# Kernel tuning notes

Measured on AMD Instinct MI355X. Metric: run time of the kernel, lower is better.

Reference implementation:

```python
import jax, jax.numpy as jnp
import numpy as np

N_NODES = 50000


def gcn_conv(x, W, b, src, dst):
    # PyG GCNConv: lin (no bias) -> add self-loops -> symmetric deg norm ->
    # scatter-add messages to target nodes -> add bias.
    n = x.shape[0]
    xw = x @ W  # [N, H]
    loops = jnp.arange(n, dtype=src.dtype)
    s = jnp.concatenate([src, loops])
    d = jnp.concatenate([dst, loops])
    deg = jax.ops.segment_sum(jnp.ones(d.shape[0], dtype=x.dtype), d, num_segments=n)
    dinv = deg ** -0.5  # deg >= 1 due to self-loops
    norm = dinv[s] * dinv[d]  # [E+N]
    msg = xw[s] * norm[:, None]  # gather + scale, [E+N, H]
    out = jax.ops.segment_sum(msg, d, num_segments=n)  # scatter-add
    return out + b


def setup_inputs() -> dict:
    key = jax.random.key(0)
    ks = jax.random.split(key, 8)
    in_feats, hidden, out_feats, p = 64, 64, 32, 4
    x = jax.random.normal(ks[0], (N_NODES, in_feats), dtype=jnp.float32)
    edge_index = jax.random.randint(ks[1], (2, 800000), 0, N_NODES, dtype=jnp.int64)
    s1 = (1.0 / in_feats) ** 0.5
    s2 = (1.0 / hidden) ** 0.5
    W1 = jax.random.uniform(ks[2], (in_feats, hidden), jnp.float32, -s1, s1)
    b1 = jnp.zeros((hidden,), jnp.float32)
    W2 = jax.random.uniform(ks[3], (hidden, hidden), jnp.float32, -s2, s2)
    b2 = jnp.zeros((hidden,), jnp.float32)
    Wr = jax.random.uniform(ks[4], (hidden, out_feats * p), jnp.float32, -s2, s2)
    br = jax.random.uniform(ks[5], (out_feats * p,), jnp.float32, -s2, s2)
    return {"x": x, "edge_index": edge_index, "W1": W1, "b1": b1,
            "W2": W2, "b2": b2, "Wr": Wr, "br": br}


def reference(x, edge_index, W1, b1, W2, b2, Wr, br):
    src, dst = edge_index[0], edge_index[1]
    h = jax.nn.relu(gcn_conv(x, W1, b1, src, dst))
    h = jax.nn.relu(gcn_conv(h, W2, b2, src, dst))
    g = jnp.mean(h, axis=0, keepdims=True)  # [1, hidden]
    out = (g @ Wr + br).reshape(32, 4)  # (out_feats, p)
    return out
```

## Files before the change

kernel.cpp:

```cpp
#include <hip/hip_runtime.h>
#include <math.h>


#define CH 4096
#define MAXNB 1024

__global__ __launch_bounds__(256) void k_bucket_hist(const int* __restrict__ dst,
                                                     int* __restrict__ histmat,
                                                     int E, int NB) {
    __shared__ int ih[MAXNB];
    int t = threadIdx.x;
    for (int k = t; k < NB; k += 256) ih[k] = 0;
    __syncthreads();
    int base = blockIdx.x * CH;
    for (int i = 0; i < CH; i += 256) {
        int e = base + i + t;
        if (e < E) atomicAdd(&ih[dst[e] >> 6], 1);
    }
    __syncthreads();
    for (int k = t; k < NB; k += 256) histmat[(size_t)blockIdx.x * NB + k] = ih[k];
}

__global__ __launch_bounds__(256) void k_colscan(int* __restrict__ histmat,
                                                 int* __restrict__ tot,
                                                 int NB, int nch) {
    int k = blockIdx.x * 256 + threadIdx.x;
    if (k >= NB) return;
    int run = 0;
    int b = 0;
    for (; b + 8 <= nch; b += 8) {
        int v[8];
#pragma unroll
        for (int u = 0; u < 8; u++) v[u] = histmat[(size_t)(b + u) * NB + k];
#pragma unroll
        for (int u = 0; u < 8; u++) {
            int x = v[u];
            histmat[(size_t)(b + u) * NB + k] = run;
            run += x;
        }
    }
    for (; b < nch; b++) {
        int x = histmat[(size_t)b * NB + k];
        histmat[(size_t)b * NB + k] = run;
        run += x;
    }
    tot[k] = run;
}

__global__ __launch_bounds__(256) void k_scanb(const int* __restrict__ tot,
                                               int* __restrict__ bstart,
                                               int* __restrict__ offsets,
                                               int NB, int E, int n) {
    __shared__ int sc[256];
    __shared__ int carry;
    int t = threadIdx.x;
    if (t == 0) carry = 0;
    __syncthreads();
    int nchunk = (NB + 255) / 256;
    for (int c = 0; c < nchunk; c++) {
        int idx = c * 256 + t;
        int v = (idx < NB) ? tot[idx] : 0;
        sc[t] = v;
        __syncthreads();
        for (int off = 1; off < 256; off <<= 1) {
            int x = (t >= off) ? sc[t - off] : 0;
            __syncthreads();
            sc[t] += x;
            __syncthreads();
        }
        if (idx < NB) bstart[idx] = sc[t] - v + carry;
        __syncthreads();
        if (t == 0) carry += sc[255];
        __syncthreads();
    }
    if (t == 0) { bstart[NB] = E; offsets[n] = E; }
}

__global__ __launch_bounds__(256) void k_bucket_scatter(const int* __restrict__ src,
                                                        const int* __restrict__ dst,
                                                        const int* __restrict__ histmat,
                                                        const int* __restrict__ bstart,
                                                        int* __restrict__ staged,
                                                        int E, int NB) {
    __shared__ int cur[MAXNB];
    int t = threadIdx.x;
    for (int k = t; k < NB; k += 256)
        cur[k] = bstart[k] + histmat[(size_t)blockIdx.x * NB + k];
    __syncthreads();
    int base = blockIdx.x * CH;
    for (int i = 0; i < CH; i += 256) {
        int e = base + i + t;
        if (e < E) {
            int d = dst[e];
            int pos = atomicAdd(&cur[d >> 6], 1);
            staged[pos] = (src[e] << 6) | (d & 63);
        }
    }
}

__global__ __launch_bounds__(256) void k_local_sort(const int* __restrict__ staged,
                                                    const int* __restrict__ bstart,
                                                    int* __restrict__ csr_src,
                                                    int* __restrict__ offsets,
                                                    float* __restrict__ dinv, int n) {
    __shared__ int cnt[64];
    __shared__ int pos[64];
    __shared__ int cur[64];
    int t = threadIdx.x;
    if (t < 64) cnt[t] = 0;
    __syncthreads();
    int k = blockIdx.x;
    int beg = bstart[k], end = bstart[k + 1];
    for (int e = beg + t; e < end; e += 256) atomicAdd(&cnt[staged[e] & 63], 1);
    __syncthreads();
    if (t == 0) {
        int run = 0;
        for (int i = 0; i < 64; i++) { pos[i] = run; run += cnt[i]; }
    }
    __syncthreads();
    if (t < 64) {
        cur[t] = pos[t];
        int node = k * 64 + t;
        if (node < n) {
            offsets[node] = beg + pos[t];
            dinv[node] = 1.0f / sqrtf((float)(cnt[t] + 1));
        }
    }
    __syncthreads();
    for (int e = beg + t; e < end; e += 256) {
        int pk = staged[e];
        int p = atomicAdd(&cur[pk & 63], 1);
        csr_src[beg + p] = pk >> 6;
    }
}

__global__ __launch_bounds__(256) void k_gemm_scale(const float* __restrict__ X,
                                                    const float* __restrict__ W,
                                                    const float* __restrict__ dinv,
                                                    float* __restrict__ Y, int n) {
    __shared__ float Ws[64 * 64];
    __shared__ float xs[16][64];
    int t = threadIdx.x, w = t >> 6, f = t & 63;
    const float4* W4 = (const float4*)W;
    float4* Ws4 = (float4*)Ws;
#pragma unroll
    for (int j = 0; j < 4; j++) Ws4[t + 256 * j] = W4[t + 256 * j];
    int r0 = blockIdx.x * 16;
#pragma unroll
    for (int i = 0; i < 4; i++) {
        int r = r0 + w * 4 + i;
        xs[w * 4 + i][f] = (r < n) ? X[(size_t)r * 64 + f] : 0.f;
    }
    __syncthreads();
    float acc[4] = {0.f, 0.f, 0.f, 0.f};
#pragma unroll 8
    for (int k = 0; k < 64; k++) {
        float wv = Ws[k * 64 + f];
#pragma unroll
        for (int i = 0; i < 4; i++) acc[i] += xs[w * 4 + i][k] * wv;
    }
#pragma unroll
    for (int i = 0; i < 4; i++) {
        int r = r0 + w * 4 + i;
        if (r < n) Y[(size_t)r * 64 + f] = dinv[r] * acc[i];
    }
}

template <bool POOL>
__global__ __launch_bounds__(256) void k_aggregate(const float* __restrict__ Y,
                                                   const float* __restrict__ dinv,
                                                   const float* __restrict__ bias,
                                                   const int* __restrict__ offsets,
                                                   const int* __restrict__ csr_src,
                                                   float* __restrict__ H,
                                                   float* __restrict__ pbuf, int n) {
    __shared__ float4 sm4[4][16];
    const float4* Y4 = (const float4*)Y;
    int t = threadIdx.x, w = t >> 6, l = t & 63;
    int q = l >> 4, c = l & 15;
    int node = blockIdx.x * 4 + w;
    bool valid = node < n;
    float4 hval = make_float4(0.f, 0.f, 0.f, 0.f);
    if (valid) {
        float4 acc = make_float4(0.f, 0.f, 0.f, 0.f);
        if (q == 0) acc = Y4[(size_t)node * 16 + c];
        int beg = offsets[node], end = offsets[node + 1];
        for (int j = beg + q; j < end; j += 16) {
#pragma unroll
            for (int u = 0; u < 4; u++) {
                int jj = j + 4 * u;
                bool ok = jj < end;
                float4 v = make_float4(0.f, 0.f, 0.f, 0.f);
                if (ok) {
                    int s = csr_src[jj];
                    v = Y4[(size_t)s * 16 + c];
                }
                acc.x += v.x; acc.y += v.y; acc.z += v.z; acc.w += v.w;
            }
        }
#pragma unroll
        for (int m = 16; m <= 32; m <<= 1) {
            acc.x += __shfl_xor(acc.x, m);
            acc.y += __shfl_xor(acc.y, m);
            acc.z += __shfl_xor(acc.z, m);
            acc.w += __shfl_xor(acc.w, m);
        }
        float dv = dinv[node];
        float4 b4 = ((const float4*)bias)[c];
        hval.x = fmaxf(dv * acc.x + b4.x, 0.f);
        hval.y = fmaxf(dv * acc.y + b4.y, 0.f);
        hval.z = fmaxf(dv * acc.z + b4.z, 0.f);
        hval.w = fmaxf(dv * acc.w + b4.w, 0.f);
        if (!POOL && q == 0) ((float4*)H)[(size_t)node * 16 + c] = hval;
    }
    if (POOL) {
        if (q == 0) sm4[w][c] = valid ? hval : make_float4(0.f, 0.f, 0.f, 0.f);
        __syncthreads();
        if (t < 16) {
            float4 a = sm4[0][t], b = sm4[1][t], d = sm4[2][t], e = sm4[3][t];
            float4 s;
            s.x = (a.x + b.x) + (d.x + e.x);
            s.y = (a.y + b.y) + (d.y + e.y);
            s.z = (a.z + b.z) + (d.z + e.z);
            s.w = (a.w + b.w) + (d.w + e.w);
            ((float4*)pbuf)[(size_t)blockIdx.x * 16 + t] = s;
        }
    }
}

__global__ void k_mean_final(const float* __restrict__ pbuf, float* __restrict__ g,
                             int nrows) {
    __shared__ float part[256];
    int t = threadIdx.x, w = t >> 6, f = t & 63;
    float local = 0.f;
    for (int r = blockIdx.x * 4 + w; r < nrows; r += gridDim.x * 4)
        local += pbuf[(size_t)r * 64 + f];
    part[t] = local;
    __syncthreads();
    if (w == 0) {
        float tot = part[f] + part[64 + f] + part[128 + f] + part[192 + f];
        atomicAdd(&g[f], tot);
    }
}

__global__ void k_readout(const float* __restrict__ g, const float* __restrict__ Wr,
                          const float* __restrict__ br, float* __restrict__ out,
                          float invn) {
    __shared__ float gl[64];
    int t = threadIdx.x;
    if (t < 64) gl[t] = g[t] * invn;
    __syncthreads();
    float acc = br[t];
#pragma unroll
    for (int k = 0; k < 64; k++) acc += gl[k] * Wr[k * 128 + t];
    out[t] = acc;
}

extern "C" void kernel_launch(void* const* d_in, const int* in_sizes, int n_in,
                              void* d_out, int out_size, void* d_ws, size_t ws_size,
                              hipStream_t stream) {
    const float* x  = (const float*)d_in[0];
    const int*   ei = (const int*)d_in[1];
    const float* W1 = (const float*)d_in[2];
    const float* b1 = (const float*)d_in[3];
    const float* W2 = (const float*)d_in[4];
    const float* b2 = (const float*)d_in[5];
    const float* Wr = (const float*)d_in[6];
    const float* br = (const float*)d_in[7];
    float* out = (float*)d_out;

    int n = in_sizes[0] / 64;
    int E = in_sizes[1] / 2;
    const int* src = ei;
    const int* dst = ei + E;

    int NB  = (n + 63) / 64;
    int nch = (E + CH - 1) / CH;

    char* p = (char*)d_ws;
    float* y = (float*)p;      p += (size_t)n * 64 * sizeof(float);
    float* h = (float*)p;      p += (size_t)n * 64 * sizeof(float);
    float* dinv = (float*)p;   p += (size_t)n * sizeof(float);
    float* g = (float*)p;      p += 64 * sizeof(float);
    int* staged = (int*)p;     p += (size_t)E * sizeof(int);
    int* csr_src = (int*)p;    p += (size_t)E * sizeof(int);
    int* offsets = (int*)p;    p += (size_t)(n + 1) * sizeof(int);
    int* histmat = (int*)p;    p += (size_t)nch * NB * sizeof(int);
    int* tot = (int*)p;        p += (size_t)NB * sizeof(int);
    int* bstart = (int*)p;     p += (size_t)(NB + 1) * sizeof(int);

    int gb = (n + 3) / 4;

    hipMemsetAsync(g, 0, 64 * sizeof(float), stream);
    k_bucket_hist<<<nch, 256, 0, stream>>>(dst, histmat, E, NB);
    k_colscan<<<(NB + 255) / 256, 256, 0, stream>>>(histmat, tot, NB, nch);
    k_scanb<<<1, 256, 0, stream>>>(tot, bstart, offsets, NB, E, n);
    k_bucket_scatter<<<nch, 256, 0, stream>>>(src, dst, histmat, bstart, staged, E, NB);
    k_local_sort<<<NB, 256, 0, stream>>>(staged, bstart, csr_src, offsets, dinv, n);

    k_gemm_scale<<<(n + 15) / 16, 256, 0, stream>>>(x, W1, dinv, y, n);
    k_aggregate<false><<<gb, 256, 0, stream>>>(y, dinv, b1, offsets, csr_src, h, nullptr, n);
    k_gemm_scale<<<(n + 15) / 16, 256, 0, stream>>>(h, W2, dinv, y, n);
    float* pbuf = h;
    k_aggregate<true><<<gb, 256, 0, stream>>>(y, dinv, b2, offsets, csr_src, nullptr, pbuf, n);

    k_mean_final<<<64, 256, 0, stream>>>(pbuf, g, gb);
    k_readout<<<1, 128, 0, stream>>>(g, Wr, br, out, 1.0f / (float)n);
}
```

Before: 231.6 us.

## Store node features in bf16 and CSR source indices as 16-bit

Intermediate feature matrices (scaled GEMM outputs and layer-1 hidden activations) are now stored as bf16 instead of fp32, while accumulation stays in fp32. CSR source indices are narrowed to 16-bit unsigned shorts. This halves the bytes moved by the gather-heavy aggregation and by the GEMM loads and stores. The cost is lost precision, and the 16-bit indices cannot represent node ids above 65535; since the later shift by 6 keeps only 16 bits, correctness depends on n staying below 65536.

```diff
diff --git a/kernel.cpp b/kernel.cpp
--- a/kernel.cpp
+++ b/kernel.cpp
@@ -4,6 +4,14 @@
 
 #define CH 4096
 #define MAXNB 1024
+
+__device__ __forceinline__ float bf2f(unsigned short u) {
+    return __uint_as_float(((unsigned)u) << 16);
+}
+__device__ __forceinline__ unsigned short f2bf(float x) {
+    unsigned b = __float_as_uint(x);
+    return (unsigned short)((b + 0x7FFF + ((b >> 16) & 1)) >> 16);
+}
 
 __global__ __launch_bounds__(256) void k_bucket_hist(const int* __restrict__ dst,
                                                      int* __restrict__ histmat,
@@ -100,7 +108,7 @@
 
 __global__ __launch_bounds__(256) void k_local_sort(const int* __restrict__ staged,
                                                     const int* __restrict__ bstart,
-                                                    int* __restrict__ csr_src,
+                                                    unsigned short* __restrict__ csr,
                                                     int* __restrict__ offsets,
                                                     float* __restrict__ dinv, int n) {
     __shared__ int cnt[64];
@@ -130,14 +138,15 @@
     for (int e = beg + t; e < end; e += 256) {
         int pk = staged[e];
         int p = atomicAdd(&cur[pk & 63], 1);
-        csr_src[beg + p] = pk >> 6;
-    }
-}
-
-__global__ __launch_bounds__(256) void k_gemm_scale(const float* __restrict__ X,
+        csr[beg + p] = (unsigned short)(pk >> 6);
+    }
+}
+
+template <bool BIN>
+__global__ __launch_bounds__(256) void k_gemm_scale(const void* __restrict__ Xv,
                                                     const float* __restrict__ W,
                                                     const float* __restrict__ dinv,
-                                                    float* __restrict__ Y, int n) {
+                                                    unsigned short* __restrict__ Y, int n) {
     __shared__ float Ws[64 * 64];
     __shared__ float xs[16][64];
     int t = threadIdx.x, w = t >> 6, f = t & 63;
@@ -149,7 +158,11 @@
 #pragma unroll
     for (int i = 0; i < 4; i++) {
         int r = r0 + w * 4 + i;
-        xs[w * 4 + i][f] = (r < n) ? X[(size_t)r * 64 + f] : 0.f;
+        float v = 0.f;
+        if (r < n)
+            v = BIN ? bf2f(((const unsigned short*)Xv)[(size_t)r * 64 + f])
+                    : ((const float*)Xv)[(size_t)r * 64 + f];
+        xs[w * 4 + i][f] = v;
     }
     __syncthreads();
     float acc[4] = {0.f, 0.f, 0.f, 0.f};
@@ -162,20 +175,20 @@
 #pragma unroll
     for (int i = 0; i < 4; i++) {
         int r = r0 + w * 4 + i;
-        if (r < n) Y[(size_t)r * 64 + f] = dinv[r] * acc[i];
+        if (r < n) Y[(size_t)r * 64 + f] = f2bf(dinv[r] * acc[i]);
     }
 }
 
 template <bool POOL>
-__global__ __launch_bounds__(256) void k_aggregate(const float* __restrict__ Y,
+__global__ __launch_bounds__(256) void k_aggregate(const unsigned short* __restrict__ Y,
                                                    const float* __restrict__ dinv,
                                                    const float* __restrict__ bias,
                                                    const int* __restrict__ offsets,
-                                                   const int* __restrict__ csr_src,
-                                                   float* __restrict__ H,
+                                                   const unsigned short* __restrict__ csr,
+                                                   unsigned short* __restrict__ H,
                                                    float* __restrict__ pbuf, int n) {
     __shared__ float4 sm4[4][16];
-    const float4* Y4 = (const float4*)Y;
+    const ushort4* Y4 = (const ushort4*)Y;
     int t = threadIdx.x, w = t >> 6, l = t & 63;
     int q = l >> 4, c = l & 15;
     int node = blockIdx.x * 4 + w;
@@ -183,19 +196,21 @@
     float4 hval = make_float4(0.f, 0.f, 0.f, 0.f);
     if (valid) {
         float4 acc = make_float4(0.f, 0.f, 0.f, 0.f);
-        if (q == 0) acc = Y4[(size_t)node * 16 + c];
+        if (q == 0) {
+            ushort4 u = Y4[(size_t)node * 16 + c];
+            acc = make_float4(bf2f(u.x), bf2f(u.y), bf2f(u.z), bf2f(u.w));
+        }
         int beg = offsets[node], end = offsets[node + 1];
         for (int j = beg + q; j < end; j += 16) {
 #pragma unroll
             for (int u = 0; u < 4; u++) {
                 int jj = j + 4 * u;
-                bool ok = jj < end;
-                float4 v = make_float4(0.f, 0.f, 0.f, 0.f);
-                if (ok) {
-                    int s = csr_src[jj];
-                    v = Y4[(size_t)s * 16 + c];
+                if (jj < end) {
+                    int s = csr[jj];
+                    ushort4 v = Y4[(size_t)s * 16 + c];
+                    acc.x += bf2f(v.x); acc.y += bf2f(v.y);
+                    acc.z += bf2f(v.z); acc.w += bf2f(v.w);
                 }
-                acc.x += v.x; acc.y += v.y; acc.z += v.z; acc.w += v.w;
             }
         }
 #pragma unroll
@@ -211,7 +226,12 @@
         hval.y = fmaxf(dv * acc.y + b4.y, 0.f);
         hval.z = fmaxf(dv * acc.z + b4.z, 0.f);
         hval.w = fmaxf(dv * acc.w + b4.w, 0.f);
-        if (!POOL && q == 0) ((float4*)H)[(size_t)node * 16 + c] = hval;
+        if (!POOL && q == 0) {
+            ushort4 o;
+            o.x = f2bf(hval.x); o.y = f2bf(hval.y);
+            o.z = f2bf(hval.z); o.w = f2bf(hval.w);
+            ((ushort4*)H)[(size_t)node * 16 + c] = o;
+        }
     }
     if (POOL) {
         if (q == 0) sm4[w][c] = valid ? hval : make_float4(0.f, 0.f, 0.f, 0.f);
@@ -278,31 +298,30 @@
     int nch = (E + CH - 1) / CH;
 
     char* p = (char*)d_ws;
-    float* y = (float*)p;      p += (size_t)n * 64 * sizeof(float);
-    float* h = (float*)p;      p += (size_t)n * 64 * sizeof(float);
+    unsigned short* y1 = (unsigned short*)p; p += (size_t)n * 64 * sizeof(unsigned short);
+    unsigned short* y2 = (unsigned short*)p; p += (size_t)n * 64 * sizeof(unsigned short);
+    float* pbuf = (float*)p;   p += (size_t)((n + 3) / 4) * 64 * sizeof(float);
     float* dinv = (float*)p;   p += (size_t)n * sizeof(float);
     float* g = (float*)p;      p += 64 * sizeof(float);
     int* staged = (int*)p;     p += (size_t)E * sizeof(int);
-    int* csr_src = (int*)p;    p += (size_t)E * sizeof(int);
     int* offsets = (int*)p;    p += (size_t)(n + 1) * sizeof(int);
     int* histmat = (int*)p;    p += (size_t)nch * NB * sizeof(int);
     int* tot = (int*)p;        p += (size_t)NB * sizeof(int);
     int* bstart = (int*)p;     p += (size_t)(NB + 1) * sizeof(int);
-
-    int gb = (n + 3) / 4;
+    unsigned short* csr = (unsigned short*)p; p += (size_t)E * sizeof(unsigned short);
 
     hipMemsetAsync(g, 0, 64 * sizeof(float), stream);
     k_bucket_hist<<<nch, 256, 0, stream>>>(dst, histmat, E, NB);
     k_colscan<<<(NB + 255) / 256, 256, 0, stream>>>(histmat, tot, NB, nch);
     k_scanb<<<1, 256, 0, stream>>>(tot, bstart, offsets, NB, E, n);
     k_bucket_scatter<<<nch, 256, 0, stream>>>(src, dst, histmat, bstart, staged, E, NB);
-    k_local_sort<<<NB, 256, 0, stream>>>(staged, bstart, csr_src, offsets, dinv, n);
-
-    k_gemm_scale<<<(n + 15) / 16, 256, 0, stream>>>(x, W1, dinv, y, n);
-    k_aggregate<false><<<gb, 256, 0, stream>>>(y, dinv, b1, offsets, csr_src, h, nullptr, n);
-    k_gemm_scale<<<(n + 15) / 16, 256, 0, stream>>>(h, W2, dinv, y, n);
-    float* pbuf = h;
-    k_aggregate<true><<<gb, 256, 0, stream>>>(y, dinv, b2, offsets, csr_src, nullptr, pbuf, n);
+    k_local_sort<<<NB, 256, 0, stream>>>(staged, bstart, csr, offsets, dinv, n);
+
+    int gb = (n + 3) / 4;
+    k_gemm_scale<false><<<(n + 15) / 16, 256, 0, stream>>>(x, W1, dinv, y1, n);
+    k_aggregate<false><<<gb, 256, 0, stream>>>(y1, dinv, b1, offsets, csr, y2, nullptr, n);
+    k_gemm_scale<true><<<(n + 15) / 16, 256, 0, stream>>>(y2, W2, dinv, y1, n);
+    k_aggregate<true><<<gb, 256, 0, stream>>>(y1, dinv, b2, offsets, csr, nullptr, pbuf, n);
 
     k_mean_final<<<64, 256, 0, stream>>>(pbuf, g, gb);
     k_readout<<<1, 128, 0, stream>>>(g, Wr, br, out, 1.0f / (float)n);
```

Measured after the change: 231.1 us. Within noise of the previous version (-0.2%).
